# Optimization experiments

Hardware: AMD Instinct MI355X
Metric: run time of the kernel (lower is better)

The kernel has to match this reference:

```python
import jax, jax.numpy as jnp
import numpy as np

D_MODEL = 768
N_HEADS = 8
HEAD_DIM = D_MODEL // N_HEADS  # 96


def setup_inputs() -> dict:
    key = jax.random.key(0)
    k1, k2, k3, k4, k5 = jax.random.split(key, 5)
    B, LQ, LK = 2, 4096, 4096
    hidden_states = jax.random.normal(k1, (B, LQ, D_MODEL), dtype=jnp.float32)
    key_value_states = jax.random.normal(k2, (B, LK, D_MODEL), dtype=jnp.float32)
    # learned projection params (initialized as eye in torch, but learned; use random here)
    Wq = jax.random.normal(k3, (D_MODEL, D_MODEL), dtype=jnp.float32) * 0.02
    Wk = jax.random.normal(k4, (D_MODEL, D_MODEL), dtype=jnp.float32) * 0.02
    Wv = jax.random.normal(k5, (D_MODEL, D_MODEL), dtype=jnp.float32) * 0.02
    return {"hidden_states": hidden_states, "key_value_states": key_value_states,
            "Wq": Wq, "Wk": Wk, "Wv": Wv}


def reference(hidden_states, key_value_states, Wq, Wk, Wv):
    B, LQ, _ = hidden_states.shape
    LK = key_value_states.shape[1]
    # linear projections (no bias)
    q = hidden_states @ Wq            # [B, LQ, D]
    k = key_value_states @ Wk         # [B, LK, D]
    v = key_value_states @ Wv         # [B, LK, D]
    # split heads: [B, H, L, d]
    def shape(x, L):
        return x.reshape(B, L, N_HEADS, HEAD_DIM).transpose(0, 2, 1, 3)
    q = shape(q, LQ) / jnp.sqrt(jnp.float32(HEAD_DIM))
    k = shape(k, LK)
    v = shape(v, LK)
    scores = jnp.einsum('bhqd,bhkd->bhqk', q, k)   # [B, H, LQ, LK]
    attn = jax.nn.softmax(scores, axis=-1)
    # dropout p=0.0 -> identity
    ctx = jnp.einsum('bhqk,bhkd->bhqd', attn, v)   # [B, H, LQ, d]
    context = ctx.transpose(0, 2, 1, 3).reshape(B, LQ, D_MODEL)
    return context
```

## Files before the change

kernel.cpp:

```cpp
#include <hip/hip_runtime.h>
#include <hip/hip_bf16.h>


typedef __bf16 bf16x8 __attribute__((ext_vector_type(8)));
typedef __bf16 bf16x4 __attribute__((ext_vector_type(4)));
typedef float  f32x4  __attribute__((ext_vector_type(4)));
typedef float  f32x16 __attribute__((ext_vector_type(16)));
typedef unsigned u32x4 __attribute__((ext_vector_type(4)));

#define DM   768
#define NH   8
#define HD   96
#define SEQ  4096
#define BATCH 2
#define WELEM (DM*DM)
#define XELEM (BATCH*SEQ*DM)

#define GLDS16(gp, lp) __builtin_amdgcn_global_load_lds( \
    (const __attribute__((address_space(1))) void*)(gp), \
    (__attribute__((address_space(3))) void*)(lp), 16, 0, 0)

__global__ __launch_bounds__(256) void transpose_w3(
    const float* __restrict__ Wq, const float* __restrict__ Wk, const float* __restrict__ Wv,
    __bf16* __restrict__ Tq, __bf16* __restrict__ Tk, __bf16* __restrict__ Tv)
{
    __shared__ __bf16 Ls[64][72];
    const int id = blockIdx.x;
    const int which = id / 144;
    const int tile = id - which * 144;
    const int ti = tile / 12, tj = tile % 12;
    const float* W = (which == 0) ? Wq : (which == 1) ? Wk : Wv;
    __bf16* T      = (which == 0) ? Tq : (which == 1) ? Tk : Tv;

    const int t = threadIdx.x;
    const int row = t >> 2, q4 = t & 3;
    const float* src = W + (size_t)(ti * 64 + row) * DM + tj * 64 + q4 * 16;
    float4 f0 = *reinterpret_cast<const float4*>(src);
    float4 f1 = *reinterpret_cast<const float4*>(src + 4);
    float4 f2 = *reinterpret_cast<const float4*>(src + 8);
    float4 f3 = *reinterpret_cast<const float4*>(src + 12);
    bf16x8 v0, v1;
    v0[0]=(__bf16)f0.x; v0[1]=(__bf16)f0.y; v0[2]=(__bf16)f0.z; v0[3]=(__bf16)f0.w;
    v0[4]=(__bf16)f1.x; v0[5]=(__bf16)f1.y; v0[6]=(__bf16)f1.z; v0[7]=(__bf16)f1.w;
    v1[0]=(__bf16)f2.x; v1[1]=(__bf16)f2.y; v1[2]=(__bf16)f2.z; v1[3]=(__bf16)f2.w;
    v1[4]=(__bf16)f3.x; v1[5]=(__bf16)f3.y; v1[6]=(__bf16)f3.z; v1[7]=(__bf16)f3.w;
    *reinterpret_cast<bf16x8*>(&Ls[row][q4 * 16])     = v0;
    *reinterpret_cast<bf16x8*>(&Ls[row][q4 * 16 + 8]) = v1;
    __syncthreads();
    #pragma unroll
    for (int j = 0; j < 2; ++j) {
        const int idx = t + j * 256;
        const int orow = idx >> 3, oc = idx & 7;
        bf16x8 o;
        #pragma unroll
        for (int e = 0; e < 8; ++e) o[e] = Ls[oc * 8 + e][orow];
        *reinterpret_cast<bf16x8*>(
            &T[(size_t)(tj * 64 + orow) * DM + ti * 64 + oc * 8]) = o;
    }
}

__global__ __launch_bounds__(256, 2) void proj_gemm128(
    const float* __restrict__ X, const __bf16* __restrict__ Wt,
    __bf16* __restrict__ Y, int mode, float scale)
{
    __shared__ __bf16 As[2][128][64];
    __shared__ __bf16 Bs[2][128][64];

    const int t = threadIdx.x;
    const int l = t & 63;
    const int w = t >> 6;
    const int ln = l & 15, g = l >> 4;
    const int wm = w >> 1, wn = w & 1;

    const int id = blockIdx.x;
    const int xcd = id & 7, c = id >> 3;
    const int m0 = (xcd * 8 + c / 6) * 128;
    const int n0 = (c % 6) * 128;

    size_t afsrc[4], bsrc[4]; unsigned awdst[4], sdst[4];
    #pragma unroll
    for (int j = 0; j < 4; ++j) {
        const int cid = j * 256 + t;
        const int r = cid >> 3, cc = cid & 7, cs = cc ^ (r & 7);
        afsrc[j] = (size_t)(m0 + r) * DM + cc * 8;
        awdst[j] = r * 128 + (cc ^ (r & 7)) * 16;
        bsrc[j]  = (size_t)(n0 + r) * DM + cs * 8;
        sdst[j]  = cid * 16;
    }

    float4 va[4][2];
    auto LOADA = [&](int kt) {
        #pragma unroll
        for (int j = 0; j < 4; ++j) {
            const float* p = X + (size_t)kt * 64 + afsrc[j];
            va[j][0] = *reinterpret_cast<const float4*>(p);
            va[j][1] = *reinterpret_cast<const float4*>(p + 4);
        }
    };
    auto WRITEA = [&](int buf) {
        #pragma unroll
        for (int j = 0; j < 4; ++j) {
            bf16x8 v;
            v[0]=(__bf16)va[j][0].x; v[1]=(__bf16)va[j][0].y;
            v[2]=(__bf16)va[j][0].z; v[3]=(__bf16)va[j][0].w;
            v[4]=(__bf16)va[j][1].x; v[5]=(__bf16)va[j][1].y;
            v[6]=(__bf16)va[j][1].z; v[7]=(__bf16)va[j][1].w;
            *reinterpret_cast<bf16x8*>((char*)As + buf * 16384 + awdst[j]) = v;
        }
    };

    f32x4 acc[4][4] = {};

    LOADA(0); WRITEA(0);
    #pragma unroll
    for (int j = 0; j < 4; ++j) GLDS16(Wt + bsrc[j], (char*)Bs + sdst[j]);
    __syncthreads();

    const int NKT = DM / 64;
    for (int kt = 0; kt < NKT; ++kt) {
        const int cur = kt & 1, nxt = cur ^ 1;
        const bool more = kt + 1 < NKT;
        if (more) {
            LOADA(kt + 1);
            const size_t k0n = (size_t)(kt + 1) * 64;
            #pragma unroll
            for (int j = 0; j < 4; ++j)
                GLDS16(Wt + k0n + bsrc[j], (char*)Bs + nxt * 16384u + sdst[j]);
        }

        #pragma unroll
        for (int kk = 0; kk < 2; ++kk) {
            bf16x8 a[4], b[4];
            #pragma unroll
            for (int ms = 0; ms < 4; ++ms) {
                const int row = wm * 64 + ms * 16 + ln;
                const int slot = (kk * 4 + g) ^ (row & 7);
                a[ms] = *reinterpret_cast<const bf16x8*>(
                    (const char*)As + cur * 16384 + row * 128 + slot * 16);
            }
            #pragma unroll
            for (int ns = 0; ns < 4; ++ns) {
                const int row = wn * 64 + ns * 16 + ln;
                const int slot = (kk * 4 + g) ^ (row & 7);
                b[ns] = *reinterpret_cast<const bf16x8*>(
                    (const char*)Bs + cur * 16384 + row * 128 + slot * 16);
            }
            #pragma unroll
            for (int ms = 0; ms < 4; ++ms)
                #pragma unroll
                for (int ns = 0; ns < 4; ++ns)
                    acc[ms][ns] = __builtin_amdgcn_mfma_f32_16x16x32_bf16(
                        a[ms], b[ns], acc[ms][ns], 0, 0, 0);
        }
        if (more) WRITEA(nxt);
        __syncthreads();
    }

    #pragma unroll
    for (int ms = 0; ms < 4; ++ms) {
        #pragma unroll
        for (int ns = 0; ns < 4; ++ns) {
            const int col = n0 + wn * 64 + ns * 16 + ln;
            const int h = col / HD, d = col - h * HD;
            const int row_base = m0 + wm * 64 + ms * 16 + 4 * g;
            if (mode == 0) {
                #pragma unroll
                for (int r = 0; r < 4; ++r) {
                    const int row = row_base + r;
                    const int b_ = row >> 12, q = row & (SEQ - 1);
                    Y[(((size_t)(b_ * NH + h) * SEQ) + q) * HD + d] =
                        (__bf16)(acc[ms][ns][r] * scale);
                }
            } else {
                const int b_ = row_base >> 12, kq = row_base & (SEQ - 1);
                bf16x4 v;
                #pragma unroll
                for (int r = 0; r < 4; ++r) v[r] = (__bf16)acc[ms][ns][r];
                *reinterpret_cast<bf16x4*>(
                    &Y[((size_t)(b_ * NH + h) * HD + d) * SEQ + kq]) = v;
            }
        }
    }
}

__global__ __launch_bounds__(256, 2) void attn_kernel(
    const __bf16* __restrict__ Q, const __bf16* __restrict__ K,
    const __bf16* __restrict__ Vt, float* __restrict__ out)
{
    __shared__ __bf16 Ks[2][64][128];
    __shared__ __bf16 Vs[3][96][64];

    const int t_ = threadIdx.x;
    const int l = t_ & 63;
    const int w = t_ >> 6;
    const int lh = l >> 5;
    const int c31 = l & 31;

    const int swz = (blockIdx.x & 7) * 64 + (blockIdx.x >> 3);
    const int bh = swz >> 5;
    const int qb = swz & 31;
    const int b = bh >> 3, hd = bh & 7;
    const int q0 = qb * 128 + w * 32;

    const size_t base = (size_t)bh * SEQ * HD;
    const __bf16* Kg = K + base;
    const __bf16* Vg = Vt + base;

    size_t ksrc[4], vsrc[3];
    unsigned kdst[4], vdst[3];
    #pragma unroll
    for (int j = 0; j < 4; ++j) {
        const int cid = (w * 4 + j) * 64 + l;
        const int r = cid >> 4, cc = cid & 15;
        int cs = cc ^ (r & 7); if (cs >= 12) cs = 0;
        ksrc[j] = (size_t)r * HD + cs * 8;
        kdst[j] = (w * 4 + j) * 1024;
    }
    #pragma unroll
    for (int j = 0; j < 3; ++j) {
        const int cid = (w * 3 + j) * 64 + l;
        const int d = cid >> 3, cc = cid & 7;
        const int cs = cc ^ (d & 7);
        vsrc[j] = (size_t)d * SEQ + cs * 8;
        vdst[j] = (w * 3 + j) * 1024;
    }

    bf16x8 qf[6];
    #pragma unroll
    for (int st = 0; st < 6; ++st)
        qf[st] = *reinterpret_cast<const bf16x8*>(
            &Q[base + (size_t)(q0 + c31) * HD + st * 16 + 8 * lh]);

    f32x16 acc[3] = {};
    f32x16 sA0, sA1, sB0, sB1;
    float l_r = 0.f;
    int vcur = 0, vst = 2;

    auto STAGE = [&](int tile, int kp, int vbuf) {
        const size_t ko = (size_t)tile * 64 * HD;
        #pragma unroll
        for (int j = 0; j < 4; ++j)
            GLDS16(Kg + ko + ksrc[j], (char*)Ks + kp * 16384 + kdst[j]);
        const size_t vo = (size_t)tile * 64;
        #pragma unroll
        for (int j = 0; j < 3; ++j)
            GLDS16(Vg + vo + vsrc[j], (char*)Vs + vbuf * 12288 + vdst[j]);
    };

    auto QKT = [&](int pbuf, f32x16& S0, f32x16& S1) {
        S0 = (f32x16){}; S1 = (f32x16){};
        #pragma unroll
        for (int st = 0; st < 6; ++st) {
            const int slot = (2 * st + lh) ^ (c31 & 7);
            bf16x8 ka0 = *reinterpret_cast<const bf16x8*>(
                (const char*)Ks + pbuf * 16384 + c31 * 256 + slot * 16);
            bf16x8 ka1 = *reinterpret_cast<const bf16x8*>(
                (const char*)Ks + pbuf * 16384 + (32 + c31) * 256 + slot * 16);
            S0 = __builtin_amdgcn_mfma_f32_32x32x16_bf16(ka0, qf[st], S0, 0, 0, 0);
            S1 = __builtin_amdgcn_mfma_f32_32x32x16_bf16(ka1, qf[st], S1, 0, 0, 0);
        }
    };

    auto SMPV = [&](f32x16& S0, f32x16& S1) {
        float p0 = 0.f, p1 = 0.f;
        #pragma unroll
        for (int r = 0; r < 16; ++r) {
            const float e0 = __builtin_amdgcn_exp2f(S0[r]);
            const float e1 = __builtin_amdgcn_exp2f(S1[r]);
            S0[r] = e0; S1[r] = e1; p0 += e0; p1 += e1;
        }
        l_r += p0 + p1;
        unsigned up[2][4][2];
        #pragma unroll
        for (int qd = 0; qd < 4; ++qd)
            #pragma unroll
            for (int j = 0; j < 2; ++j) {
                asm("v_cvt_pk_bf16_f32 %0, %1, %2"
                    : "=v"(up[0][qd][j])
                    : "v"(S0[4 * qd + 2 * j]), "v"(S0[4 * qd + 2 * j + 1]));
                asm("v_cvt_pk_bf16_f32 %0, %1, %2"
                    : "=v"(up[1][qd][j])
                    : "v"(S1[4 * qd + 2 * j]), "v"(S1[4 * qd + 2 * j + 1]));
            }
        const unsigned vbo = vcur * 12288;
        #pragma unroll
        for (int kc = 0; kc < 4; ++kc) {
            const int ks = kc >> 1, cp = kc & 1;
            unsigned x0 = up[ks][2 * cp][0],     x1 = up[ks][2 * cp][1];
            unsigned y0 = up[ks][2 * cp + 1][0], y1 = up[ks][2 * cp + 1][1];
            asm("v_permlane32_swap_b32 %0, %1" : "+v"(x0), "+v"(y0));
            asm("v_permlane32_swap_b32 %0, %1" : "+v"(x1), "+v"(y1));
            u32x4 pw; pw[0] = x0; pw[1] = x1; pw[2] = y0; pw[3] = y1;
            const bf16x8 pa = __builtin_bit_cast(bf16x8, pw);
            __builtin_amdgcn_s_setprio(1);
            #pragma unroll
            for (int dt = 0; dt < 3; ++dt) {
                const int dd = dt * 32 + c31;
                const int slot = (2 * kc + lh) ^ (dd & 7);
                bf16x8 vb = *reinterpret_cast<const bf16x8*>(
                    (const char*)Vs + vbo + dd * 128 + slot * 16);
                acc[dt] = __builtin_amdgcn_mfma_f32_32x32x16_bf16(pa, vb, acc[dt], 0, 0, 0);
            }
            __builtin_amdgcn_s_setprio(0);
        }
        vcur = (vcur == 2) ? 0 : vcur + 1;
        vst  = (vst  == 2) ? 0 : vst  + 1;
    };

    STAGE(0, 0, 0);
    __syncthreads();
    STAGE(1, 1, 1);
    QKT(0, sA0, sA1);

    const int NT = SEQ / 64;
    for (int u2 = 0; u2 < NT / 2; ++u2) {
        const int u = 2 * u2;
        __syncthreads();
        if (u + 2 < NT) STAGE(u + 2, 0, vst);
        QKT(1, sB0, sB1);
        SMPV(sA0, sA1);
        __syncthreads();
        if (u + 3 < NT) STAGE(u + 3, 1, vst);
        if (u + 2 < NT) QKT(0, sA0, sA1);
        SMPV(sB0, sB1);
    }

    {
        float ex = l_r;
        asm volatile("" : "+v"(ex));
        asm("v_permlane32_swap_b32 %0, %1" : "+v"(ex), "+v"(l_r));
        l_r += ex;
    }
    const float inv = 1.0f / l_r;
    #pragma unroll
    for (int r = 0; r < 16; ++r) {
        const int ql = (r & 3) + 8 * (r >> 2) + 4 * lh;
        const float ir = __shfl(inv, ql, 64);
        const int q = q0 + ql;
        float* dst = out + ((size_t)(b * SEQ + q)) * DM + hd * HD;
        #pragma unroll
        for (int dt = 0; dt < 3; ++dt)
            dst[dt * 32 + c31] = acc[dt][r] * ir;
    }
}

extern "C" void kernel_launch(void* const* d_in, const int* in_sizes, int n_in,
                              void* d_out, int out_size, void* d_ws, size_t ws_size,
                              hipStream_t stream) {
    const float* hidden = (const float*)d_in[0];
    const float* kv     = (const float*)d_in[1];
    const float* Wq     = (const float*)d_in[2];
    const float* Wk     = (const float*)d_in[3];
    const float* Wv     = (const float*)d_in[4];
    float* out = (float*)d_out;

    __bf16* Wt_q = (__bf16*)d_ws;
    __bf16* Wt_k = Wt_q + WELEM;
    __bf16* Wt_v = Wt_k + WELEM;
    __bf16* Qb   = Wt_v + WELEM;
    __bf16* Kb   = Qb + XELEM;
    __bf16* Vtb  = Kb + XELEM;

    transpose_w3<<<432, 256, 0, stream>>>(Wq, Wk, Wv, Wt_q, Wt_k, Wt_v);

    const float qscale = 0.10206207261596575f * 1.4426950408889634f;
    proj_gemm128<<<384, 256, 0, stream>>>(hidden, Wt_q, Qb,  0, qscale);
    proj_gemm128<<<384, 256, 0, stream>>>(kv,     Wt_k, Kb,  0, 1.0f);
    proj_gemm128<<<384, 256, 0, stream>>>(kv,     Wt_v, Vtb, 1, 1.0f);

    attn_kernel<<<512, 256, 0, stream>>>(Qb, Kb, Vtb, out);
}
```

Before: 194.6 us.

## Pre-convert inputs to bf16 and merge three projection GEMMs into one launch

Adds a conversion kernel that turns hidden and kv activations into bf16, staged in the output buffer as scratch, so the projection GEMM can load A tiles with direct global-to-LDS loads instead of fp32 register loads plus conversion. The three Q/K/V projection launches are merged into a single 1152-block launch that picks its operand set from the block index, removing two launch tails and filling the GPU better. The attention QK^T loop now seeds the first MFMA with a preallocated zero accumulator instead of zeroing S each tile. The cost is an extra pass over the activations in memory and reliance on the output buffer being large enough to hold both bf16 copies before attention overwrites it.

```diff
diff --git a/kernel.cpp b/kernel.cpp
--- a/kernel.cpp
+++ b/kernel.cpp
@@ -59,9 +59,26 @@
     }
 }
 
-__global__ __launch_bounds__(256, 2) void proj_gemm128(
-    const float* __restrict__ X, const __bf16* __restrict__ Wt,
-    __bf16* __restrict__ Y, int mode, float scale)
+__global__ __launch_bounds__(256) void convert_x(
+    const float* __restrict__ X0, const float* __restrict__ X1,
+    __bf16* __restrict__ Y0, __bf16* __restrict__ Y1)
+{
+    const float* X = blockIdx.y ? X1 : X0;
+    __bf16* Y      = blockIdx.y ? Y1 : Y0;
+    const size_t i = ((size_t)blockIdx.x * 256 + threadIdx.x) * 8;
+    float4 lo = *reinterpret_cast<const float4*>(X + i);
+    float4 hi = *reinterpret_cast<const float4*>(X + i + 4);
+    bf16x8 v;
+    v[0]=(__bf16)lo.x; v[1]=(__bf16)lo.y; v[2]=(__bf16)lo.z; v[3]=(__bf16)lo.w;
+    v[4]=(__bf16)hi.x; v[5]=(__bf16)hi.y; v[6]=(__bf16)hi.z; v[7]=(__bf16)hi.w;
+    *reinterpret_cast<bf16x8*>(Y + i) = v;
+}
+
+__global__ __launch_bounds__(256, 2) void proj_all(
+    const __bf16* __restrict__ Xh, const __bf16* __restrict__ Xkv,
+    const __bf16* __restrict__ Wtq, const __bf16* __restrict__ Wtk,
+    const __bf16* __restrict__ Wtv, __bf16* __restrict__ Yq,
+    __bf16* __restrict__ Yk, __bf16* __restrict__ Yv, float qscale)
 {
     __shared__ __bf16 As[2][128][64];
     __shared__ __bf16 Bs[2][128][64];
@@ -72,60 +89,48 @@
     const int ln = l & 15, g = l >> 4;
     const int wm = w >> 1, wn = w & 1;
 
-    const int id = blockIdx.x;
-    const int xcd = id & 7, c = id >> 3;
+    const int id3 = blockIdx.x;
+    const int xcd = id3 & 7;
+    const int u = id3 >> 3;
+    const int which = u % 3;
+    const int c = u / 3;
     const int m0 = (xcd * 8 + c / 6) * 128;
     const int n0 = (c % 6) * 128;
 
-    size_t afsrc[4], bsrc[4]; unsigned awdst[4], sdst[4];
+    const __bf16* Xb = (which == 0) ? Xh : Xkv;
+    const __bf16* Wt = (which == 0) ? Wtq : (which == 1) ? Wtk : Wtv;
+    __bf16* Y        = (which == 0) ? Yq : (which == 1) ? Yk : Yv;
+    const int mode   = (which == 2) ? 1 : 0;
+    const float scale = (which == 0) ? qscale : 1.0f;
+
+    size_t asrc[4], bsrc[4]; unsigned sdst[4];
     #pragma unroll
     for (int j = 0; j < 4; ++j) {
         const int cid = j * 256 + t;
         const int r = cid >> 3, cc = cid & 7, cs = cc ^ (r & 7);
-        afsrc[j] = (size_t)(m0 + r) * DM + cc * 8;
-        awdst[j] = r * 128 + (cc ^ (r & 7)) * 16;
-        bsrc[j]  = (size_t)(n0 + r) * DM + cs * 8;
-        sdst[j]  = cid * 16;
-    }
-
-    float4 va[4][2];
-    auto LOADA = [&](int kt) {
-        #pragma unroll
-        for (int j = 0; j < 4; ++j) {
-            const float* p = X + (size_t)kt * 64 + afsrc[j];
-            va[j][0] = *reinterpret_cast<const float4*>(p);
-            va[j][1] = *reinterpret_cast<const float4*>(p + 4);
-        }
-    };
-    auto WRITEA = [&](int buf) {
-        #pragma unroll
-        for (int j = 0; j < 4; ++j) {
-            bf16x8 v;
-            v[0]=(__bf16)va[j][0].x; v[1]=(__bf16)va[j][0].y;
-            v[2]=(__bf16)va[j][0].z; v[3]=(__bf16)va[j][0].w;
-            v[4]=(__bf16)va[j][1].x; v[5]=(__bf16)va[j][1].y;
-            v[6]=(__bf16)va[j][1].z; v[7]=(__bf16)va[j][1].w;
-            *reinterpret_cast<bf16x8*>((char*)As + buf * 16384 + awdst[j]) = v;
-        }
-    };
+        asrc[j] = (size_t)(m0 + r) * DM + cs * 8;
+        bsrc[j] = (size_t)(n0 + r) * DM + cs * 8;
+        sdst[j] = cid * 16;
+    }
 
     f32x4 acc[4][4] = {};
 
-    LOADA(0); WRITEA(0);
+    #pragma unroll
+    for (int j = 0; j < 4; ++j) GLDS16(Xb + asrc[j], (char*)As + sdst[j]);
     #pragma unroll
     for (int j = 0; j < 4; ++j) GLDS16(Wt + bsrc[j], (char*)Bs + sdst[j]);
     __syncthreads();
 
     const int NKT = DM / 64;
     for (int kt = 0; kt < NKT; ++kt) {
-        const int cur = kt & 1, nxt = cur ^ 1;
-        const bool more = kt + 1 < NKT;
-        if (more) {
-            LOADA(kt + 1);
+        const int cur = kt & 1;
+        if (kt + 1 < NKT) {
+            const unsigned nb = (cur ^ 1) * 16384u;
             const size_t k0n = (size_t)(kt + 1) * 64;
             #pragma unroll
-            for (int j = 0; j < 4; ++j)
-                GLDS16(Wt + k0n + bsrc[j], (char*)Bs + nxt * 16384u + sdst[j]);
+            for (int j = 0; j < 4; ++j) GLDS16(Xb + k0n + asrc[j], (char*)As + nb + sdst[j]);
+            #pragma unroll
+            for (int j = 0; j < 4; ++j) GLDS16(Wt + k0n + bsrc[j], (char*)Bs + nb + sdst[j]);
         }
 
         #pragma unroll
@@ -152,7 +157,6 @@
                     acc[ms][ns] = __builtin_amdgcn_mfma_f32_16x16x32_bf16(
                         a[ms], b[ns], acc[ms][ns], 0, 0, 0);
         }
-        if (more) WRITEA(nxt);
         __syncthreads();
     }
 
@@ -235,6 +239,8 @@
     f32x16 sA0, sA1, sB0, sB1;
     float l_r = 0.f;
     int vcur = 0, vst = 2;
+    f32x16 ZC = {};
+    asm volatile("" : "+v"(ZC));
 
     auto STAGE = [&](int tile, int kp, int vbuf) {
         const size_t ko = (size_t)tile * 64 * HD;
@@ -248,7 +254,6 @@
     };
 
     auto QKT = [&](int pbuf, f32x16& S0, f32x16& S1) {
-        S0 = (f32x16){}; S1 = (f32x16){};
         #pragma unroll
         for (int st = 0; st < 6; ++st) {
             const int slot = (2 * st + lh) ^ (c31 & 7);
@@ -256,8 +261,10 @@
                 (const char*)Ks + pbuf * 16384 + c31 * 256 + slot * 16);
             bf16x8 ka1 = *reinterpret_cast<const bf16x8*>(
                 (const char*)Ks + pbuf * 16384 + (32 + c31) * 256 + slot * 16);
-            S0 = __builtin_amdgcn_mfma_f32_32x32x16_bf16(ka0, qf[st], S0, 0, 0, 0);
-            S1 = __builtin_amdgcn_mfma_f32_32x32x16_bf16(ka1, qf[st], S1, 0, 0, 0);
+            S0 = __builtin_amdgcn_mfma_f32_32x32x16_bf16(ka0, qf[st],
+                     st == 0 ? ZC : S0, 0, 0, 0);
+            S1 = __builtin_amdgcn_mfma_f32_32x32x16_bf16(ka1, qf[st],
+                     st == 0 ? ZC : S1, 0, 0, 0);
         }
     };
 
@@ -361,12 +368,15 @@
     __bf16* Kb   = Qb + XELEM;
     __bf16* Vtb  = Kb + XELEM;
 
+    __bf16* Xh_bf  = (__bf16*)d_out;
+    __bf16* Xkv_bf = Xh_bf + XELEM;
+
     transpose_w3<<<432, 256, 0, stream>>>(Wq, Wk, Wv, Wt_q, Wt_k, Wt_v);
+    convert_x<<<dim3(XELEM / 8 / 256, 2), 256, 0, stream>>>(hidden, kv, Xh_bf, Xkv_bf);
 
     const float qscale = 0.10206207261596575f * 1.4426950408889634f;
-    proj_gemm128<<<384, 256, 0, stream>>>(hidden, Wt_q, Qb,  0, qscale);
-    proj_gemm128<<<384, 256, 0, stream>>>(kv,     Wt_k, Kb,  0, 1.0f);
-    proj_gemm128<<<384, 256, 0, stream>>>(kv,     Wt_v, Vtb, 1, 1.0f);
+    proj_all<<<1152, 256, 0, stream>>>(Xh_bf, Xkv_bf, Wt_q, Wt_k, Wt_v,
+                                       Qb, Kb, Vtb, qscale);
 
     attn_kernel<<<512, 256, 0, stream>>>(Qb, Kb, Vtb, out);
 }
```

Result: faster. 183.5 us (-5.7%).
